# Kernel optimization log

Hardware: AMD Instinct MI355X
Metric: run time of the kernel (lower is better)

## Reference

```python
import jax, jax.numpy as jnp
import numpy as np

LEAKY_ALPHA = 0.2  # tf.nn.leaky_relu default


def setup_inputs() -> dict:
    key = jax.random.key(0)
    ks = jax.random.split(key, 8)
    N, F_IN, OUT, E = 100000, 256, 64, 1600000
    x = jax.random.normal(ks[0], (1, N, F_IN), dtype=jnp.float32)
    W = jax.random.normal(ks[1], (F_IN, OUT), dtype=jnp.float32) * 0.05
    a1 = jax.random.normal(ks[2], (OUT, 1), dtype=jnp.float32) * 0.1
    b1 = jnp.zeros((1,), dtype=jnp.float32)
    a2 = jax.random.normal(ks[3], (OUT, 1), dtype=jnp.float32) * 0.1
    b2 = jnp.zeros((1,), dtype=jnp.float32)
    out_bias = jnp.zeros((OUT,), dtype=jnp.float32)
    edge_src = jax.random.randint(ks[4], (E,), 0, N, dtype=jnp.int32)
    edge_dst = jax.random.randint(ks[5], (E,), 0, N, dtype=jnp.int32)
    return {"x": x, "W": W, "a1": a1, "b1": b1, "a2": a2, "b2": b2,
            "out_bias": out_bias, "edge_src": edge_src, "edge_dst": edge_dst,
            "nb_nodes": N}


def reference(x, W, a1, b1, a2, b2, out_bias, edge_src, edge_dst, nb_nodes):
    N = int(nb_nodes)
    h = jnp.einsum('nf,fo->no', x[0], W)          # [N, out_sz] projected features
    f1 = (h @ a1 + b1)[:, 0]                       # [N] per-node src score
    f2 = (h @ a2 + b2)[:, 0]                       # [N] per-node dst score
    # edge logits: f1[src] + f2[dst], leaky relu
    e = jax.nn.leaky_relu(f1[edge_src] + f2[edge_dst], negative_slope=LEAKY_ALPHA)
    # row-wise sparse softmax over edges grouped by src
    m = jax.ops.segment_max(e, edge_src, num_segments=N)
    m = jnp.where(jnp.isfinite(m), m, 0.0)
    ex = jnp.exp(e - m[edge_src])
    denom = jax.ops.segment_sum(ex, edge_src, num_segments=N)
    coefs = ex / denom[edge_src]                   # [E]
    # spmm: aggregate neighbor features
    vals = jax.ops.segment_sum(coefs[:, None] * h[edge_dst], edge_src, num_segments=N)
    ret = jax.nn.elu(vals + out_bias)              # bias_add + elu act
    return ret[None]                               # [1, N, out_sz]
```

## Files before the change

### kernel.cpp

```cpp
#include <hip/hip_runtime.h>
#include <math.h>

#define F_IN 256
#define OUT  64
#define LEAKY 0.2f
#define BSH  9
#define BSZ  512
#define CAP  12288

typedef __attribute__((ext_vector_type(4))) float f32x4;
typedef __attribute__((ext_vector_type(8))) __bf16 bf16x8;
typedef __attribute__((ext_vector_type(4))) unsigned int u32x4;

__device__ __forceinline__ unsigned cvt_pk_bf16(float lo, float hi) {
    unsigned r;
    asm volatile("v_cvt_pk_bf16_f32 %0, %1, %2" : "=v"(r) : "v"(lo), "v"(hi));
    return r;
}

__device__ __forceinline__ void gload_lds16(const float* g, float* l) {
    __builtin_amdgcn_global_load_lds((const __attribute__((address_space(1))) void*)g,
                                     (__attribute__((address_space(3))) void*)l, 16, 0, 0);
}

__global__ __launch_bounds__(256) void fused_part_gemm_kernel(
    const float* __restrict__ x, const float* __restrict__ W,
    const float* __restrict__ a1, const float* __restrict__ b1,
    const float* __restrict__ a2, const float* __restrict__ b2,
    unsigned short* __restrict__ h2, float* __restrict__ f1, float* __restrict__ f2,
    const int* __restrict__ esrc, const int* __restrict__ edst,
    int* __restrict__ gcur, unsigned* __restrict__ ebkt,
    int N, int E, int nPart, int gemmBlocks)
{
    __shared__ __align__(16) unsigned int Wt[64 * 128];
    __shared__ __align__(16) float xs[4][2][1024];

    const int bid = blockIdx.x;
    const int t   = threadIdx.x;
    const int r   = bid % 3;

    if (r == 2) {
        int c = bid / 3;
        if (c >= nPart) return;
        int* hist = (int*)&xs[0][0][0];
        int* run  = hist + 256;
        int* off  = hist + 512;
        hist[t] = 0; off[t] = 0;
        __syncthreads();
        const int e0 = c * 4096;
#pragma unroll
        for (int k = 0; k < 4; ++k) {
            int i = e0 + k * 1024 + t * 4;
            if (i + 4 <= E) {
                int4 s = *(const int4*)&esrc[i];
                atomicAdd(&hist[s.x >> BSH], 1);
                atomicAdd(&hist[s.y >> BSH], 1);
                atomicAdd(&hist[s.z >> BSH], 1);
                atomicAdd(&hist[s.w >> BSH], 1);
            } else {
                for (int e = i; e < E; ++e) atomicAdd(&hist[esrc[e] >> BSH], 1);
            }
        }
        __syncthreads();
        if (hist[t] > 0) run[t] = t * CAP + atomicAdd(&gcur[t], hist[t]);
        __syncthreads();
#pragma unroll
        for (int k = 0; k < 4; ++k) {
            int i = e0 + k * 1024 + t * 4;
#pragma unroll
            for (int q = 0; q < 4; ++q) {
                int e = i + q;
                if (e < E) {
                    int s = esrc[e];
                    int d = edst[e];
                    int b = s >> BSH;
                    int l = atomicAdd(&off[b], 1);
                    ebkt[run[b] + l] = (unsigned)d | ((unsigned)(s & (BSZ - 1)) << 17);
                }
            }
        }
        return;
    }

    const int g    = (bid / 3) * 2 + r;
    if (g >= gemmBlocks) return;
    const int wave = t >> 6;
    const int lane = t & 63;
    const int rowB = g * 128;

    for (int p = t; p < 64 * 32; p += 256) {
        int c = p & 63, gg = p >> 6;
        float f[8];
#pragma unroll
        for (int j = 0; j < 8; ++j) f[j] = W[(gg * 8 + j) * 64 + c];
        u32x4 d;
        d.x = cvt_pk_bf16(f[0], f[1]);
        d.y = cvt_pk_bf16(f[2], f[3]);
        d.z = cvt_pk_bf16(f[4], f[5]);
        d.w = cvt_pk_bf16(f[6], f[7]);
        int gs = gg ^ (c & 7);
        *(u32x4*)&Wt[c * 128 + gs * 4] = d;
    }

    auto stage = [&](int buf, int kc) {
#pragma unroll
        for (int i = 0; i < 4; ++i) {
            int lrow = i * 8 + (lane >> 3);
            int gg   = lane & 7;
            int srow = rowB + wave * 32 + lrow; if (srow > N - 1) srow = N - 1;
            int gsw  = gg ^ (lrow & 7);
            const float* src = x + (size_t)srow * F_IN + kc + gsw * 4;
            gload_lds16(src, &xs[wave][buf][i * 256]);
        }
    };

    f32x4 acc[2][4];
#pragma unroll
    for (int m = 0; m < 2; ++m)
#pragma unroll
        for (int n = 0; n < 4; ++n) acc[m][n] = (f32x4){0.f, 0.f, 0.f, 0.f};

    stage(0, 0);
    __syncthreads();

#pragma unroll 1
    for (int ks = 0; ks < 8; ++ks) {
        const int cur = ks & 1;
        if (ks < 7) {
            stage(cur ^ 1, (ks + 1) * 32);
            asm volatile("s_waitcnt vmcnt(4)" ::: "memory");
        } else {
            asm volatile("s_waitcnt vmcnt(0)" ::: "memory");
        }
        __builtin_amdgcn_sched_barrier(0);

        bf16x8 bfrag[4];
#pragma unroll
        for (int ns = 0; ns < 4; ++ns) {
            int c = ns * 16 + (lane & 15);
            int G = ks * 4 + (lane >> 4);
            u32x4 bw = *(u32x4*)&Wt[c * 128 + ((G ^ (c & 7)) << 2)];
            bfrag[ns] = __builtin_bit_cast(bf16x8, bw);
        }
#pragma unroll
        for (int ms = 0; ms < 2; ++ms) {
            int lrow = ms * 16 + (lane & 15);
            int g0   = (lane >> 4) * 2;
            float4 xa = *(float4*)&xs[wave][cur][lrow * 32 + (((g0 + 0) ^ (lrow & 7)) << 2)];
            float4 xb = *(float4*)&xs[wave][cur][lrow * 32 + (((g0 + 1) ^ (lrow & 7)) << 2)];
            u32x4 ad;
            ad.x = cvt_pk_bf16(xa.x, xa.y);
            ad.y = cvt_pk_bf16(xa.z, xa.w);
            ad.z = cvt_pk_bf16(xb.x, xb.y);
            ad.w = cvt_pk_bf16(xb.z, xb.w);
            bf16x8 afrag = __builtin_bit_cast(bf16x8, ad);
#pragma unroll
            for (int ns = 0; ns < 4; ++ns)
                acc[ms][ns] = __builtin_amdgcn_mfma_f32_16x16x32_bf16(afrag, bfrag[ns],
                                                                      acc[ms][ns], 0, 0, 0);
        }
    }

    float A1v[4], A2v[4];
#pragma unroll
    for (int ns = 0; ns < 4; ++ns) {
        A1v[ns] = a1[ns * 16 + (lane & 15)];
        A2v[ns] = a2[ns * 16 + (lane & 15)];
    }
    float B1 = b1[0], B2 = b2[0];
#pragma unroll
    for (int ms = 0; ms < 2; ++ms) {
#pragma unroll
        for (int rr = 0; rr < 4; ++rr) {
            int grow = rowB + wave * 32 + ms * 16 + ((lane >> 4) << 2) + rr;
            float s1 = 0.f, s2 = 0.f;
#pragma unroll
            for (int ns = 0; ns < 4; ++ns) {
                float v = acc[ms][ns][rr];
                if (grow < N)
                    h2[(size_t)grow * OUT + ns * 16 + (lane & 15)] =
                        (unsigned short)(cvt_pk_bf16(v, v) & 0xffffu);
                s1 += v * A1v[ns];
                s2 += v * A2v[ns];
            }
#pragma unroll
            for (int off = 1; off < 16; off <<= 1) {
                s1 += __shfl_xor(s1, off);
                s2 += __shfl_xor(s2, off);
            }
            if ((lane & 15) == 0 && grow < N) { f1[grow] = s1 + B1; f2[grow] = s2 + B2; }
        }
    }
}

__global__ __launch_bounds__(256) void csr_build_kernel(
    const unsigned* __restrict__ ebkt, const int* __restrict__ gcur,
    int* __restrict__ counts, int* __restrict__ row_start,
    int* __restrict__ csr4, int N)
{
    __shared__ int cnt[BSZ];
    __shared__ int cur[BSZ];
    __shared__ int sc[2][BSZ];
    const int b = blockIdx.x;
    const int t = threadIdx.x;

    cnt[t] = 0; cnt[t + 256] = 0;
    __syncthreads();

    const int e0 = b * CAP;
    const int e1 = e0 + gcur[b];
    for (int i = e0 + t; i < e1; i += 256)
        atomicAdd(&cnt[ebkt[i] >> 17], 1);
    __syncthreads();

    sc[0][t] = cnt[t]; sc[0][t + 256] = cnt[t + 256];
    __syncthreads();
    int srcb = 0;
    for (int d = 1; d < BSZ; d <<= 1) {
        int dstb = srcb ^ 1;
        int i0 = t, i1 = t + 256;
        sc[dstb][i0] = sc[srcb][i0] + (i0 >= d ? sc[srcb][i0 - d] : 0);
        sc[dstb][i1] = sc[srcb][i1] + (i1 >= d ? sc[srcb][i1 - d] : 0);
        __syncthreads();
        srcb = dstb;
    }

    const int nodeBase = b << BSH;
#pragma unroll
    for (int j = 0; j < 2; ++j) {
        int i = t + j * 256;
        int excl = sc[srcb][i] - cnt[i];
        cur[i] = excl;
        int gn = nodeBase + i;
        if (gn < N) {
            row_start[gn] = e0 + excl;
            counts[gn]    = cnt[i];
        }
    }
    __syncthreads();

    for (int i = e0 + t; i < e1; i += 256) {
        unsigned w = ebkt[i];
        int ls = w >> 17;
        int pos = e0 + atomicAdd(&cur[ls], 1);
        csr4[pos] = (int)(w & 0x1FFFFu);
    }
}

__global__ __launch_bounds__(256) void aggregate_kernel(
    const unsigned short* __restrict__ h2, const float* __restrict__ f1,
    const float* __restrict__ f2,
    const int* __restrict__ row_start, const int* __restrict__ counts,
    const int* __restrict__ csr4, const float* __restrict__ out_bias,
    float* __restrict__ out, int N)
{
    const int t    = threadIdx.x;
    const int lane = t & 63;
    const int gl   = lane & 15;
    const int gb   = lane & 48;
    const int gw   = blockIdx.x * 16 + ((t >> 6) << 2) + (lane >> 4);
    if (gw >= N) return;

    const int base  = row_start[gw];
    const int deg   = counts[gw];
    const float f1n = f1[gw];

    float den = 0.f;
    float a0 = 0.f, a1f = 0.f, a2f = 0.f, a3f = 0.f;

    for (int c0 = 0; c0 < deg; c0 += 16) {
        int  idx   = c0 + gl;
        bool valid = idx < deg;
        int   d = valid ? csr4[base + idx] : 0;
        float e = f1n + f2[d];
        e = (e > 0.f) ? e : LEAKY * e;
        float p = valid ? __expf(e) : 0.f;
        den += p;

        unsigned pack = ((unsigned)d << 15) | (cvt_pk_bf16(p, p) & 0x7FFFu);

        int lim = deg - c0; if (lim > 16) lim = 16;
        int j = 0;
        for (; j + 2 <= lim; j += 2) {
            unsigned pk0 = __shfl((int)pack, gb + j);
            unsigned pk1 = __shfl((int)pack, gb + j + 1);
            uint2 u0 = *(const uint2*)&h2[((pk0 >> 15) << 6) + (gl << 2)];
            uint2 u1 = *(const uint2*)&h2[((pk1 >> 15) << 6) + (gl << 2)];
            float p0 = __builtin_bit_cast(float, (pk0 & 0x7FFFu) << 16);
            float p1 = __builtin_bit_cast(float, (pk1 & 0x7FFFu) << 16);
            a0  += p0 * __builtin_bit_cast(float, u0.x << 16)
                 + p1 * __builtin_bit_cast(float, u1.x << 16);
            a1f += p0 * __builtin_bit_cast(float, u0.x & 0xFFFF0000u)
                 + p1 * __builtin_bit_cast(float, u1.x & 0xFFFF0000u);
            a2f += p0 * __builtin_bit_cast(float, u0.y << 16)
                 + p1 * __builtin_bit_cast(float, u1.y << 16);
            a3f += p0 * __builtin_bit_cast(float, u0.y & 0xFFFF0000u)
                 + p1 * __builtin_bit_cast(float, u1.y & 0xFFFF0000u);
        }
        if (j < lim) {
            unsigned pk = __shfl((int)pack, gb + j);
            uint2 u = *(const uint2*)&h2[((pk >> 15) << 6) + (gl << 2)];
            float pp = __builtin_bit_cast(float, (pk & 0x7FFFu) << 16);
            a0  += pp * __builtin_bit_cast(float, u.x << 16);
            a1f += pp * __builtin_bit_cast(float, u.x & 0xFFFF0000u);
            a2f += pp * __builtin_bit_cast(float, u.y << 16);
            a3f += pp * __builtin_bit_cast(float, u.y & 0xFFFF0000u);
        }
    }

    den += __shfl_xor(den, 1);
    den += __shfl_xor(den, 2);
    den += __shfl_xor(den, 4);
    den += __shfl_xor(den, 8);

    float rd = (deg > 0) ? (1.f / den) : 0.f;
    float4 bias = *(const float4*)&out_bias[gl << 2];
    float v0 = a0  * rd + bias.x;
    float v1 = a1f * rd + bias.y;
    float v2 = a2f * rd + bias.z;
    float v3 = a3f * rd + bias.w;
    v0 = (v0 > 0.f) ? v0 : (__expf(v0) - 1.f);
    v1 = (v1 > 0.f) ? v1 : (__expf(v1) - 1.f);
    v2 = (v2 > 0.f) ? v2 : (__expf(v2) - 1.f);
    v3 = (v3 > 0.f) ? v3 : (__expf(v3) - 1.f);
    float4 res = {v0, v1, v2, v3};
    *(float4*)&out[((unsigned)gw << 6) + (gl << 2)] = res;
}

extern "C" void kernel_launch(void* const* d_in, const int* in_sizes, int n_in,
                              void* d_out, int out_size, void* d_ws, size_t ws_size,
                              hipStream_t stream)
{
    const float* x        = (const float*)d_in[0];
    const float* W        = (const float*)d_in[1];
    const float* a1       = (const float*)d_in[2];
    const float* b1       = (const float*)d_in[3];
    const float* a2       = (const float*)d_in[4];
    const float* b2       = (const float*)d_in[5];
    const float* out_bias = (const float*)d_in[6];
    const int*   esrc     = (const int*)d_in[7];
    const int*   edst     = (const int*)d_in[8];
    const int N = in_sizes[0] / F_IN;
    const int E = in_sizes[7];
    float* out = (float*)d_out;

    char* wsp = (char*)d_ws;
    size_t off = 0;
    auto alloc = [&](size_t bytes) -> void* {
        void* p = wsp + off;
        off = (off + bytes + 255) & ~(size_t)255;
        return p;
    };
    const int nbk = (N + BSZ - 1) >> BSH;

    unsigned short* h2 = (unsigned short*)alloc((size_t)N * OUT * sizeof(unsigned short));
    float* f1          = (float*)alloc((size_t)N * sizeof(float));
    float* f2          = (float*)alloc((size_t)N * sizeof(float));
    int*   counts      = (int*)alloc((size_t)N * sizeof(int));
    int*   row_start   = (int*)alloc((size_t)N * sizeof(int));
    int*   gcur        = (int*)alloc(256 * sizeof(int));
    unsigned* ebkt     = (unsigned*)alloc((size_t)nbk * CAP * sizeof(unsigned));
    int*   csr4        = (int*)alloc((size_t)nbk * CAP * sizeof(int));

    const int nPart      = (E + 4095) / 4096;
    const int gemmBlocks = (N + 127) / 128;
    int nGroup = (gemmBlocks + 1) / 2;
    if (nPart > nGroup) nGroup = nPart;

    hipMemsetAsync(gcur, 0, 256 * sizeof(int), stream);

    fused_part_gemm_kernel<<<nGroup * 3, 256, 0, stream>>>(
        x, W, a1, b1, a2, b2, h2, f1, f2, esrc, edst, gcur, ebkt, N, E, nPart, gemmBlocks);
    csr_build_kernel<<<nbk, 256, 0, stream>>>(ebkt, gcur, counts, row_start, csr4, N);
    aggregate_kernel<<<(N + 15) / 16, 256, 0, stream>>>(h2, f1, f2, row_start, counts, csr4,
                                                        out_bias, out, N);
}
```

Baseline: 109.2 us.

## Move edge score and softmax denominator into CSR build, smaller partition chunks

Edge logits, exp and per-row denominators are now computed in the CSR build kernel, which holds f1 in LDS and stores a packed dst+bf16 weight per edge plus a reciprocal denominator per node. The aggregate kernel then skips the f2 gather, the exp and the shuffle reduction. The partition blocks now handle 2048 edges each and keep src/dst in registers instead of reloading them, and blocks are interleaved 1:1 with GEMM blocks. The cost is LDS float atomics and extra work in the 196-block CSR kernel, which may serialise on hot rows.

```diff
diff --git a/kernel.cpp b/kernel.cpp
--- a/kernel.cpp
+++ b/kernel.cpp
@@ -37,52 +37,60 @@
 
     const int bid = blockIdx.x;
     const int t   = threadIdx.x;
-    const int r   = bid % 3;
-
-    if (r == 2) {
-        int c = bid / 3;
+
+    if (bid & 1) {
+        int c = bid >> 1;
         if (c >= nPart) return;
         int* hist = (int*)&xs[0][0][0];
         int* run  = hist + 256;
         int* off  = hist + 512;
         hist[t] = 0; off[t] = 0;
         __syncthreads();
-        const int e0 = c * 4096;
-#pragma unroll
-        for (int k = 0; k < 4; ++k) {
+        const int e0 = c * 2048;
+        int ss[8], dd[8], bb[8];
+#pragma unroll
+        for (int k = 0; k < 2; ++k) {
             int i = e0 + k * 1024 + t * 4;
             if (i + 4 <= E) {
-                int4 s = *(const int4*)&esrc[i];
-                atomicAdd(&hist[s.x >> BSH], 1);
-                atomicAdd(&hist[s.y >> BSH], 1);
-                atomicAdd(&hist[s.z >> BSH], 1);
-                atomicAdd(&hist[s.w >> BSH], 1);
+                int4 s4 = *(const int4*)&esrc[i];
+                int4 d4 = *(const int4*)&edst[i];
+                ss[k * 4 + 0] = s4.x; ss[k * 4 + 1] = s4.y;
+                ss[k * 4 + 2] = s4.z; ss[k * 4 + 3] = s4.w;
+                dd[k * 4 + 0] = d4.x; dd[k * 4 + 1] = d4.y;
+                dd[k * 4 + 2] = d4.z; dd[k * 4 + 3] = d4.w;
+#pragma unroll
+                for (int q = 0; q < 4; ++q) {
+                    bb[k * 4 + q] = ss[k * 4 + q] >> BSH;
+                    atomicAdd(&hist[bb[k * 4 + q]], 1);
+                }
             } else {
-                for (int e = i; e < E; ++e) atomicAdd(&hist[esrc[e] >> BSH], 1);
+#pragma unroll
+                for (int q = 0; q < 4; ++q) {
+                    int e = i + q;
+                    if (e < E) {
+                        ss[k * 4 + q] = esrc[e];
+                        dd[k * 4 + q] = edst[e];
+                        bb[k * 4 + q] = ss[k * 4 + q] >> BSH;
+                        atomicAdd(&hist[bb[k * 4 + q]], 1);
+                    } else bb[k * 4 + q] = -1;
+                }
             }
         }
         __syncthreads();
         if (hist[t] > 0) run[t] = t * CAP + atomicAdd(&gcur[t], hist[t]);
         __syncthreads();
 #pragma unroll
-        for (int k = 0; k < 4; ++k) {
-            int i = e0 + k * 1024 + t * 4;
-#pragma unroll
-            for (int q = 0; q < 4; ++q) {
-                int e = i + q;
-                if (e < E) {
-                    int s = esrc[e];
-                    int d = edst[e];
-                    int b = s >> BSH;
-                    int l = atomicAdd(&off[b], 1);
-                    ebkt[run[b] + l] = (unsigned)d | ((unsigned)(s & (BSZ - 1)) << 17);
-                }
+        for (int k = 0; k < 8; ++k) {
+            if (bb[k] >= 0) {
+                int l = atomicAdd(&off[bb[k]], 1);
+                ebkt[run[bb[k]] + l] = (unsigned)dd[k] |
+                                       ((unsigned)(ss[k] & (BSZ - 1)) << 17);
             }
         }
         return;
     }
 
-    const int g    = (bid / 3) * 2 + r;
+    const int g    = bid >> 1;
     if (g >= gemmBlocks) return;
     const int wave = t >> 6;
     const int lane = t & 63;
@@ -195,16 +203,26 @@
 
 __global__ __launch_bounds__(256) void csr_build_kernel(
     const unsigned* __restrict__ ebkt, const int* __restrict__ gcur,
-    int* __restrict__ counts, int* __restrict__ row_start,
+    const float* __restrict__ f1, const float* __restrict__ f2,
+    int* __restrict__ counts, int* __restrict__ row_start, float* __restrict__ rden,
     int* __restrict__ csr4, int N)
 {
-    __shared__ int cnt[BSZ];
-    __shared__ int cur[BSZ];
-    __shared__ int sc[2][BSZ];
+    __shared__ int   cnt[BSZ];
+    __shared__ int   cur[BSZ];
+    __shared__ int   sc[2][BSZ];
+    __shared__ float f1l[BSZ];
+    __shared__ float denl[BSZ];
     const int b = blockIdx.x;
     const int t = threadIdx.x;
+    const int nodeBase = b << BSH;
 
     cnt[t] = 0; cnt[t + 256] = 0;
+    denl[t] = 0.f; denl[t + 256] = 0.f;
+    {
+        int gn0 = nodeBase + t, gn1 = nodeBase + t + 256;
+        f1l[t]       = (gn0 < N) ? f1[gn0] : 0.f;
+        f1l[t + 256] = (gn1 < N) ? f1[gn1] : 0.f;
+    }
     __syncthreads();
 
     const int e0 = b * CAP;
@@ -225,7 +243,6 @@
         srcb = dstb;
     }
 
-    const int nodeBase = b << BSH;
 #pragma unroll
     for (int j = 0; j < 2; ++j) {
         int i = t + j * 256;
@@ -242,15 +259,28 @@
     for (int i = e0 + t; i < e1; i += 256) {
         unsigned w = ebkt[i];
         int ls = w >> 17;
+        int d  = (int)(w & 0x1FFFFu);
+        float e = f1l[ls] + f2[d];
+        e = (e > 0.f) ? e : LEAKY * e;
+        float p = __expf(e);
+        atomicAdd(&denl[ls], p);
         int pos = e0 + atomicAdd(&cur[ls], 1);
-        csr4[pos] = (int)(w & 0x1FFFFu);
+        csr4[pos] = (int)(((unsigned)d << 15) | (cvt_pk_bf16(p, p) & 0x7FFFu));
+    }
+    __syncthreads();
+
+#pragma unroll
+    for (int j = 0; j < 2; ++j) {
+        int i = t + j * 256;
+        int gn = nodeBase + i;
+        if (gn < N) rden[gn] = (cnt[i] > 0) ? (1.f / denl[i]) : 0.f;
     }
 }
 
 __global__ __launch_bounds__(256) void aggregate_kernel(
-    const unsigned short* __restrict__ h2, const float* __restrict__ f1,
-    const float* __restrict__ f2,
+    const unsigned short* __restrict__ h2,
     const int* __restrict__ row_start, const int* __restrict__ counts,
+    const float* __restrict__ rden,
     const int* __restrict__ csr4, const float* __restrict__ out_bias,
     float* __restrict__ out, int N)
 {
@@ -261,23 +291,14 @@
     const int gw   = blockIdx.x * 16 + ((t >> 6) << 2) + (lane >> 4);
     if (gw >= N) return;
 
-    const int base  = row_start[gw];
-    const int deg   = counts[gw];
-    const float f1n = f1[gw];
-
-    float den = 0.f;
+    const int base = row_start[gw];
+    const int deg  = counts[gw];
+
     float a0 = 0.f, a1f = 0.f, a2f = 0.f, a3f = 0.f;
 
     for (int c0 = 0; c0 < deg; c0 += 16) {
-        int  idx   = c0 + gl;
-        bool valid = idx < deg;
-        int   d = valid ? csr4[base + idx] : 0;
-        float e = f1n + f2[d];
-        e = (e > 0.f) ? e : LEAKY * e;
-        float p = valid ? __expf(e) : 0.f;
-        den += p;
-
-        unsigned pack = ((unsigned)d << 15) | (cvt_pk_bf16(p, p) & 0x7FFFu);
+        int idx = c0 + gl;
+        unsigned pack = (idx < deg) ? (unsigned)csr4[base + idx] : 0u;
 
         int lim = deg - c0; if (lim > 16) lim = 16;
         int j = 0;
@@ -308,12 +329,7 @@
         }
     }
 
-    den += __shfl_xor(den, 1);
-    den += __shfl_xor(den, 2);
-    den += __shfl_xor(den, 4);
-    den += __shfl_xor(den, 8);
-
-    float rd = (deg > 0) ? (1.f / den) : 0.f;
+    float rd = rden[gw];
     float4 bias = *(const float4*)&out_bias[gl << 2];
     float v0 = a0  * rd + bias.x;
     float v1 = a1f * rd + bias.y;
@@ -358,20 +374,22 @@
     float* f2          = (float*)alloc((size_t)N * sizeof(float));
     int*   counts      = (int*)alloc((size_t)N * sizeof(int));
     int*   row_start   = (int*)alloc((size_t)N * sizeof(int));
+    float* rden        = (float*)alloc((size_t)N * sizeof(float));
     int*   gcur        = (int*)alloc(256 * sizeof(int));
     unsigned* ebkt     = (unsigned*)alloc((size_t)nbk * CAP * sizeof(unsigned));
     int*   csr4        = (int*)alloc((size_t)nbk * CAP * sizeof(int));
 
-    const int nPart      = (E + 4095) / 4096;
+    const int nPart      = (E + 2047) / 2048;
     const int gemmBlocks = (N + 127) / 128;
-    int nGroup = (gemmBlocks + 1) / 2;
+    int nGroup = gemmBlocks;
     if (nPart > nGroup) nGroup = nPart;
 
     hipMemsetAsync(gcur, 0, 256 * sizeof(int), stream);
 
-    fused_part_gemm_kernel<<<nGroup * 3, 256, 0, stream>>>(
+    fused_part_gemm_kernel<<<nGroup * 2, 256, 0, stream>>>(
         x, W, a1, b1, a2, b2, h2, f1, f2, esrc, edst, gcur, ebkt, N, E, nPart, gemmBlocks);
-    csr_build_kernel<<<nbk, 256, 0, stream>>>(ebkt, gcur, counts, row_start, csr4, N);
-    aggregate_kernel<<<(N + 15) / 16, 256, 0, stream>>>(h2, f1, f2, row_start, counts, csr4,
+    csr_build_kernel<<<nbk, 256, 0, stream>>>(ebkt, gcur, f1, f2, counts, row_start, rden,
+                                              csr4, N);
+    aggregate_kernel<<<(N + 15) / 16, 256, 0, stream>>>(h2, row_start, counts, rden, csr4,
                                                         out_bias, out, N);
 }
```

Result: slower. 122.2 us (+11.9%).
